# Kernel tuning notes

Measured on AMD Instinct MI355X. Metric: run time of the kernel, lower is better.

The kernel has to match this reference:

```python
import jax, jax.numpy as jnp
import numpy as np

EPS = 1e-5  # BatchNorm eps
K = 10      # knn neighbors

def mish(x):
    return x * jnp.tanh(jax.nn.softplus(x))

def block(h, w, g, b, m, v):
    # 1x1 conv (no bias) + BN (inference stats) + Mish; h: [..., Cin], w: [Cout, Cin]
    y = jnp.einsum('...c,oc->...o', h, w)
    y = (y - m) * (g * jax.lax.rsqrt(v + EPS)) + b
    return mish(y)

def graph_feature(xt, k):
    # xt: [B, N, C] -> edge features [B, N, k, 2C] = cat(neighbor - center, center)
    xx = jnp.sum(xt * xt, axis=-1)                       # [B,N]
    inner = jnp.einsum('bnc,bmc->bnm', xt, xt)           # [B,N,N]
    neg_dist = 2.0 * inner - xx[:, :, None] - xx[:, None, :]
    idx = jax.lax.top_k(neg_dist, k)[1]                  # [B,N,k] nearest (incl. self)
    feat = jax.vmap(lambda a, i: a[i])(xt, idx)          # [B,N,k,C]
    center = jnp.broadcast_to(xt[:, :, None, :], feat.shape)
    return jnp.concatenate([feat - center, center], axis=-1)

def _bn_params(key, c):
    k1, k2, k3, k4 = jax.random.split(key, 4)
    g = 1.0 + 0.1 * jax.random.normal(k1, (c,), jnp.float32)
    b = 0.1 * jax.random.normal(k2, (c,), jnp.float32)
    m = 0.1 * jax.random.normal(k3, (c,), jnp.float32)
    v = 0.5 + jax.random.uniform(k4, (c,), jnp.float32)
    return g, b, m, v

def setup_inputs() -> dict:
    key = jax.random.key(0)
    B, C, N = 4, 3, 4096
    emb = 1024
    ks = jax.random.split(key, 20)
    d = {'x': jax.random.normal(ks[0], (B, C, N), jnp.float32)}
    dims = {'1': (64, 2 * C), '2': (64, 64), '3': (64, 128), '4': (64, 64),
            '6': (emb, 128), '7': (512, emb + 128), '8': (256, 512)}
    i = 1
    for name, (co, ci) in dims.items():
        d['w' + name] = jax.random.normal(ks[i], (co, ci), jnp.float32) * (1.0 / np.sqrt(ci))
        g, b, m, v = _bn_params(ks[i + 1], co)
        d['g' + name], d['b' + name], d['m' + name], d['v' + name] = g, b, m, v
        i += 2
    d['w9'] = jax.random.normal(ks[i], (2, 256), jnp.float32) * (1.0 / np.sqrt(256))
    return d

def reference(x, w1, g1, b1, m1, v1, w2, g2, b2, m2, v2, w3, g3, b3, m3, v3,
              w4, g4, b4, m4, v4, w6, g6, b6, m6, v6, w7, g7, b7, m7, v7,
              w8, g8, b8, m8, v8, w9):
    B, C, N = x.shape
    xt = jnp.transpose(x, (0, 2, 1))                    # [B,N,3]
    ef = graph_feature(xt, K)                           # [B,N,k,6]
    h = block(block(ef, w1, g1, b1, m1, v1), w2, g2, b2, m2, v2)
    x1 = jnp.max(h, axis=2)                             # [B,N,64]
    ef = graph_feature(x1, K)                           # [B,N,k,128]
    h = block(block(ef, w3, g3, b3, m3, v3), w4, g4, b4, m4, v4)
    x2 = jnp.max(h, axis=2)                             # [B,N,64]
    cat = jnp.concatenate([x1, x2], axis=-1)            # [B,N,128]
    h6 = block(cat, w6, g6, b6, m6, v6)                 # [B,N,1024]
    gmax = jnp.max(h6, axis=1, keepdims=True)           # [B,1,1024]
    gb = jnp.broadcast_to(gmax, (B, N, gmax.shape[-1]))
    cat2 = jnp.concatenate([gb, x1, x2], axis=-1)       # [B,N,1152]
    h = block(block(cat2, w7, g7, b7, m7, v7), w8, g8, b8, m8, v8)
    out = jnp.einsum('bnc,oc->bon', h, w9)              # [B,2,N]
    return out
```

## Files before the change

kernel.cpp:

```cpp
#include <hip/hip_runtime.h>
#include <cfloat>


#define BN_EPS 1e-5f

__device__ __forceinline__ float mish_f(float x) {
  float e = __expf(x);
  float num = e * (e + 2.0f);
  float r = x * (num / (num + 2.0f));
  return (x > 44.0f) ? x : r;
}

__device__ __forceinline__ float rl_f(float v, int l) {
  return __uint_as_float((unsigned)__builtin_amdgcn_readlane((int)__float_as_uint(v), l));
}

__device__ __forceinline__ unsigned enc_f(float f) {
  unsigned b = __float_as_uint(f);
  return (b & 0x80000000u) ? ~b : (b | 0x80000000u);
}
__device__ __forceinline__ float dec_f(unsigned u) {
  unsigned b = (u & 0x80000000u) ? (u ^ 0x80000000u) : ~u;
  return __uint_as_float(b);
}

__device__ __forceinline__ void topk_insert(float (&v)[10], int (&id)[10], float nd, int m) {
  if (nd > v[9]) {
    v[9] = nd; id[9] = m;
#pragma unroll
    for (int j = 9; j > 0; --j) {
      if (v[j] > v[j - 1]) {
        float tv = v[j]; v[j] = v[j - 1]; v[j - 1] = tv;
        int ti = id[j]; id[j] = id[j - 1]; id[j - 1] = ti;
      }
    }
  }
}

__global__ __launch_bounds__(256) void knn1_k(const float* __restrict__ x, int* __restrict__ idx1) {
  __shared__ float pls[3][4100];
  const int tid = threadIdx.x;
  const int rowBase = blockIdx.x * 64;
  const int b = rowBase >> 12;
  const float* xb = x + (size_t)b * 3 * 4096;
#pragma unroll
  for (int c = 0; c < 3; ++c) {
#pragma unroll
    for (int s = 0; s < 16; ++s) {
      int li = tid + 256 * s;
      pls[c][(li >> 10) * 1025 + (li & 1023)] = xb[c * 4096 + li];
    }
  }
  __syncthreads();
  const int sub = tid & 3;
  const int nloc = (rowBase & 4095) + (tid >> 2);
  float pnx = xb[nloc], pny = xb[4096 + nloc], pnz = xb[8192 + nloc];
  float xxn = pnx * pnx; xxn = fmaf(pny, pny, xxn); xxn = fmaf(pnz, pnz, xxn);
  float v[10]; int id[10];
#pragma unroll
  for (int j = 0; j < 10; ++j) { v[j] = -FLT_MAX; id[j] = -1; }
  const int base = sub * 1025;
  for (int i = 0; i < 1024; ++i) {
    float mx = pls[0][base + i], my = pls[1][base + i], mz = pls[2][base + i];
    float in = mx * pnx; in = fmaf(my, pny, in); in = fmaf(mz, pnz, in);
    float xm = mx * mx;  xm = fmaf(my, my, xm);  xm = fmaf(mz, mz, xm);
    float nd = 2.0f * in - xxn - xm;
    topk_insert(v, id, nd, sub * 1024 + i);
  }
  int k0 = -1, k1 = -1, k2 = -1;
#pragma unroll
  for (int r = 0; r < 10; ++r) {
    float mv = v[0]; int mi = id[0];
    { float ov = __shfl_xor(mv, 1); int oi = __shfl_xor(mi, 1);
      if (ov > mv || (ov == mv && oi < mi)) { mv = ov; mi = oi; } }
    { float ov = __shfl_xor(mv, 2); int oi = __shfl_xor(mi, 2);
      if (ov > mv || (ov == mv && oi < mi)) { mv = ov; mi = oi; } }
    if (id[0] == mi) {
#pragma unroll
      for (int j = 0; j < 9; ++j) { v[j] = v[j + 1]; id[j] = id[j + 1]; }
      v[9] = -FLT_MAX; id[9] = -1;
    }
    if ((r & 3) == sub) { if (r < 4) k0 = mi; else if (r < 8) k1 = mi; else k2 = mi; }
  }
  const int obase = (rowBase + (tid >> 2)) * 10;
  if (sub == 0)      { idx1[obase + 0] = k0; idx1[obase + 4] = k1; idx1[obase + 8] = k2; }
  else if (sub == 1) { idx1[obase + 1] = k0; idx1[obase + 5] = k1; idx1[obase + 9] = k2; }
  else if (sub == 2) { idx1[obase + 2] = k0; idx1[obase + 6] = k1; }
  else               { idx1[obase + 3] = k0; idx1[obase + 7] = k1; }
}

__global__ __launch_bounds__(256) void pre1_k(const float* __restrict__ x, const float* __restrict__ w1,
                                              float* __restrict__ e1m, float* __restrict__ e1n) {
  int gt = blockIdx.x * 256 + threadIdx.x;
  int pt = gt >> 6, c = gt & 63;
  int b = pt >> 12, n = pt & 4095;
  const float* xb = x + (size_t)b * 3 * 4096;
  float px = xb[n], py = xb[4096 + n], pz = xb[8192 + n];
  const float* wr = w1 + c * 6;
  float a0 = wr[0], a1 = wr[1], a2 = wr[2], b0 = wr[3], b1 = wr[4], b2 = wr[5];
  float vm = a0 * px; vm = fmaf(a1, py, vm); vm = fmaf(a2, pz, vm);
  float un = (b0 - a0) * px; un = fmaf(b1 - a1, py, un); un = fmaf(b2 - a2, pz, un);
  e1m[(size_t)pt * 64 + c] = vm;
  e1n[(size_t)pt * 64 + c] = un;
}

template <bool WRITE_XX>
__global__ __launch_bounds__(256) void edge_k(
    const int* __restrict__ idx,
    const float* __restrict__ vm, const float* __restrict__ un, int stride,
    const float* __restrict__ w,
    const float* __restrict__ ga, const float* __restrict__ ba, const float* __restrict__ ma, const float* __restrict__ va,
    const float* __restrict__ gb, const float* __restrict__ bb, const float* __restrict__ mb, const float* __restrict__ vb,
    float* __restrict__ outCat, int outOff, float* __restrict__ xxOut) {
  const int tid = threadIdx.x;
  const int wid = tid >> 6, lane = tid & 63;
  const int r = blockIdx.x * 4 + wid;
  const int mbase = (r >> 12) << 12;
  float4 wv[16];
  const float4* wp = (const float4*)(w + lane * 64);
#pragma unroll
  for (int i = 0; i < 16; ++i) wv[i] = wp[i];
  float s1 = ga[lane] * rsqrtf(va[lane] + BN_EPS); float t1 = ba[lane] - ma[lane] * s1;
  float s2 = gb[lane] * rsqrtf(vb[lane] + BN_EPS); float t2 = bb[lane] - mb[lane] * s2;
  float uc = un[(size_t)r * stride + lane];
  float best = -FLT_MAX;
#pragma unroll
  for (int kk = 0; kk < 10; ++kk) {
    int m = idx[r * 10 + kk];
    float pre = vm[(size_t)(mbase + m) * stride + lane] + uc;
    float h1 = mish_f(fmaf(pre, s1, t1));
    float acc = 0.f;
#pragma unroll
    for (int j4 = 0; j4 < 16; ++j4) {
      float4 wq = wv[j4];
      acc = fmaf(wq.x, rl_f(h1, 4 * j4 + 0), acc);
      acc = fmaf(wq.y, rl_f(h1, 4 * j4 + 1), acc);
      acc = fmaf(wq.z, rl_f(h1, 4 * j4 + 2), acc);
      acc = fmaf(wq.w, rl_f(h1, 4 * j4 + 3), acc);
    }
    float h2 = mish_f(fmaf(acc, s2, t2));
    best = fmaxf(best, h2);
  }
  outCat[(size_t)r * 128 + outOff + lane] = best;
  if (WRITE_XX) {
    float q = best * best;
#pragma unroll
    for (int o = 1; o < 64; o <<= 1) q += __shfl_xor(q, o);
    if (lane == 0) xxOut[r] = q;
  }
}

#define KNN2_CHUNKS 16
__global__ __launch_bounds__(256, 4) void knn2_k(const float* __restrict__ cat,
                                                 const float* __restrict__ xx2,
                                                 float* __restrict__ pv, int* __restrict__ pi) {
  __shared__ float tile[128 * 68];
  __shared__ float xxm[128];
  const int tid = threadIdx.x;
  const int r = blockIdx.x * 256 + tid;
  const int nbase = (r >> 12) << 12;
  const int cb = blockIdx.y * 256;
  float4 q[16];
  const float4* qp = (const float4*)(cat + (size_t)r * 128);
#pragma unroll
  for (int s = 0; s < 16; ++s) q[s] = qp[s];
  const float xxA = xx2[r];
  float v[10]; int id[10];
#pragma unroll
  for (int j = 0; j < 10; ++j) { v[j] = -FLT_MAX; id[j] = -1; }
  for (int t = 0; t < 2; ++t) {
    __syncthreads();
    {
      const int m = tid >> 1, h = tid & 1;
      const float4* src = (const float4*)(cat + (size_t)(nbase + cb + t * 128 + m) * 128) + h * 8;
      float4* dst = (float4*)(tile + m * 68) + h * 8;
#pragma unroll
      for (int s = 0; s < 8; ++s) dst[s] = src[s];
      if (tid < 128) xxm[tid] = xx2[nbase + cb + t * 128 + tid];
    }
    __syncthreads();
    for (int m = 0; m < 128; ++m) {
      const float4* crow = (const float4*)(tile + m * 68);
      float a0 = 0.f, a1 = 0.f, a2 = 0.f, a3 = 0.f;
#pragma unroll
      for (int c4 = 0; c4 < 16; c4 += 4) {
        float4 t0 = crow[c4 + 0], t1 = crow[c4 + 1], t2 = crow[c4 + 2], t3 = crow[c4 + 3];
        a0 = fmaf(t0.x, q[c4 + 0].x, a0); a0 = fmaf(t0.y, q[c4 + 0].y, a0);
        a0 = fmaf(t0.z, q[c4 + 0].z, a0); a0 = fmaf(t0.w, q[c4 + 0].w, a0);
        a1 = fmaf(t1.x, q[c4 + 1].x, a1); a1 = fmaf(t1.y, q[c4 + 1].y, a1);
        a1 = fmaf(t1.z, q[c4 + 1].z, a1); a1 = fmaf(t1.w, q[c4 + 1].w, a1);
        a2 = fmaf(t2.x, q[c4 + 2].x, a2); a2 = fmaf(t2.y, q[c4 + 2].y, a2);
        a2 = fmaf(t2.z, q[c4 + 2].z, a2); a2 = fmaf(t2.w, q[c4 + 2].w, a2);
        a3 = fmaf(t3.x, q[c4 + 3].x, a3); a3 = fmaf(t3.y, q[c4 + 3].y, a3);
        a3 = fmaf(t3.z, q[c4 + 3].z, a3); a3 = fmaf(t3.w, q[c4 + 3].w, a3);
      }
      float nd = 2.0f * ((a0 + a1) + (a2 + a3)) - xxA - xxm[m];
      topk_insert(v, id, nd, cb + t * 128 + m);
    }
  }
  const size_t ob = ((size_t)blockIdx.y * 16384 + r) * 10;
#pragma unroll
  for (int j = 0; j < 10; ++j) { pv[ob + j] = v[j]; pi[ob + j] = id[j]; }
}

__global__ __launch_bounds__(256) void knn2m_k(const float* __restrict__ pv,
                                               const int* __restrict__ pi,
                                               int* __restrict__ idx2) {
  const int r = blockIdx.x * 256 + threadIdx.x;
  float v[10]; int id[10];
#pragma unroll
  for (int j = 0; j < 10; ++j) { v[j] = -FLT_MAX; id[j] = -1; }
  for (int c = 0; c < KNN2_CHUNKS; ++c) {
    const size_t base = ((size_t)c * 16384 + r) * 10;
    if (pv[base] > v[9]) {
#pragma unroll
      for (int j = 0; j < 10; ++j) topk_insert(v, id, pv[base + j], pi[base + j]);
    }
  }
#pragma unroll
  for (int j = 0; j < 10; ++j) idx2[r * 10 + j] = id[j];
}

__global__ void w3s_k(const float* __restrict__ w3, float* __restrict__ w3s) {
  int t = blockIdx.x * 256 + threadIdx.x;
  int c = t >> 6, k = t & 63;
  float v;
  if (c < 64) v = w3[c * 128 + k];
  else { int cc = c - 64; v = w3[cc * 128 + 64 + k] - w3[cc * 128 + k]; }
  w3s[t] = v;
}

template <int QM, int QN, int EPI>
__global__ __launch_bounds__(256) void gemm_k(
    const float* __restrict__ A, int lda,
    const float* __restrict__ W, int ldw,
    float* __restrict__ C, int ldc, int K, int Ntot,
    const float* __restrict__ eg, const float* __restrict__ eb,
    const float* __restrict__ em, const float* __restrict__ ev,
    const float* __restrict__ pbBias, unsigned int* __restrict__ gmaxOut) {
  constexpr int BM = 64 * QM, BN = 64 * QN;
  __shared__ float aL[16][BM];
  __shared__ float bL[16][BN];
  __shared__ unsigned int cm[BN];
  const int tid = threadIdx.x;
  const int tm = tid >> 4, tn = tid & 15;
  const int rowBase = blockIdx.x * BM;
  const int colBase = blockIdx.y * BN;
  float acc[QM][QN][4][4] = {};
  if (EPI == 2 && tid < BN) cm[tid] = 0u;
  const int nkt = K >> 4;
  for (int kt = 0; kt < nkt; ++kt) {
#pragma unroll
    for (int s = 0; s < QM; ++s) {
      int fi = tid + 256 * s;
      int m = fi >> 2, k4 = fi & 3;
      float4 t4 = *(const float4*)(A + (size_t)(rowBase + m) * lda + (kt << 4) + k4 * 4);
      aL[k4 * 4 + 0][m] = t4.x; aL[k4 * 4 + 1][m] = t4.y;
      aL[k4 * 4 + 2][m] = t4.z; aL[k4 * 4 + 3][m] = t4.w;
    }
#pragma unroll
    for (int s = 0; s < QN; ++s) {
      int fi = tid + 256 * s;
      int n = fi >> 2, k4 = fi & 3;
      float4 t4 = *(const float4*)(W + (size_t)(colBase + n) * ldw + (kt << 4) + k4 * 4);
      bL[k4 * 4 + 0][n] = t4.x; bL[k4 * 4 + 1][n] = t4.y;
      bL[k4 * 4 + 2][n] = t4.z; bL[k4 * 4 + 3][n] = t4.w;
    }
    __syncthreads();
#pragma unroll
    for (int k = 0; k < 16; ++k) {
      float ar[QM][4], br[QN][4];
#pragma unroll
      for (int q = 0; q < QM; ++q) {
        float4 t4 = *(const float4*)&aL[k][q * 64 + tm * 4];
        ar[q][0] = t4.x; ar[q][1] = t4.y; ar[q][2] = t4.z; ar[q][3] = t4.w;
      }
#pragma unroll
      for (int q = 0; q < QN; ++q) {
        float4 t4 = *(const float4*)&bL[k][q * 64 + tn * 4];
        br[q][0] = t4.x; br[q][1] = t4.y; br[q][2] = t4.z; br[q][3] = t4.w;
      }
#pragma unroll
      for (int qm = 0; qm < QM; ++qm)
#pragma unroll
        for (int qn = 0; qn < QN; ++qn)
#pragma unroll
          for (int i = 0; i < 4; ++i)
#pragma unroll
            for (int j = 0; j < 4; ++j)
              acc[qm][qn][i][j] = fmaf(ar[qm][i], br[qn][j], acc[qm][qn][i][j]);
    }
    __syncthreads();
  }
  if (EPI == 0) {
#pragma unroll
    for (int qm = 0; qm < QM; ++qm)
#pragma unroll
      for (int i = 0; i < 4; ++i) {
        int row = rowBase + qm * 64 + tm * 4 + i;
#pragma unroll
        for (int qn = 0; qn < QN; ++qn) {
          float4 o;
          o.x = acc[qm][qn][i][0]; o.y = acc[qm][qn][i][1];
          o.z = acc[qm][qn][i][2]; o.w = acc[qm][qn][i][3];
          *(float4*)(C + (size_t)row * ldc + colBase + qn * 64 + tn * 4) = o;
        }
      }
  } else {
    const int bidx = rowBase >> 12;
    float sc[QN][4], sh[QN][4];
#pragma unroll
    for (int qn = 0; qn < QN; ++qn)
#pragma unroll
      for (int j = 0; j < 4; ++j) {
        int cg = colBase + qn * 64 + tn * 4 + j;
        float s = eg[cg] * rsqrtf(ev[cg] + BN_EPS);
        sc[qn][j] = s;
        sh[qn][j] = (EPI == 3) ? pbBias[bidx * Ntot + cg] : (eb[cg] - em[cg] * s);
      }
    if (EPI == 2) {
      float cmax[QN][4];
#pragma unroll
      for (int qn = 0; qn < QN; ++qn)
#pragma unroll
        for (int j = 0; j < 4; ++j) cmax[qn][j] = -FLT_MAX;
#pragma unroll
      for (int qm = 0; qm < QM; ++qm)
#pragma unroll
        for (int qn = 0; qn < QN; ++qn)
#pragma unroll
          for (int i = 0; i < 4; ++i)
#pragma unroll
            for (int j = 0; j < 4; ++j) {
              float vv = mish_f(fmaf(acc[qm][qn][i][j], sc[qn][j], sh[qn][j]));
              cmax[qn][j] = fmaxf(cmax[qn][j], vv);
            }
#pragma unroll
      for (int qn = 0; qn < QN; ++qn)
#pragma unroll
        for (int j = 0; j < 4; ++j)
          atomicMax(&cm[qn * 64 + tn * 4 + j], enc_f(cmax[qn][j]));
      __syncthreads();
      if (tid < BN) atomicMax(&gmaxOut[bidx * Ntot + colBase + tid], cm[tid]);
    } else {
#pragma unroll
      for (int qm = 0; qm < QM; ++qm)
#pragma unroll
        for (int i = 0; i < 4; ++i) {
          int row = rowBase + qm * 64 + tm * 4 + i;
#pragma unroll
          for (int qn = 0; qn < QN; ++qn) {
            float4 o;
            o.x = mish_f(fmaf(acc[qm][qn][i][0], sc[qn][0], sh[qn][0]));
            o.y = mish_f(fmaf(acc[qm][qn][i][1], sc[qn][1], sh[qn][1]));
            o.z = mish_f(fmaf(acc[qm][qn][i][2], sc[qn][2], sh[qn][2]));
            o.w = mish_f(fmaf(acc[qm][qn][i][3], sc[qn][3], sh[qn][3]));
            *(float4*)(C + (size_t)row * ldc + colBase + qn * 64 + tn * 4) = o;
          }
        }
    }
  }
}

__global__ __launch_bounds__(256) void bias7_k(const unsigned int* __restrict__ gmaxU,
                                               const float* __restrict__ w7,
                                               const float* __restrict__ g7, const float* __restrict__ b7,
                                               const float* __restrict__ m7, const float* __restrict__ v7,
                                               float* __restrict__ bias7) {
  __shared__ float gl[1024];
  const int tid = threadIdx.x;
  const int batch = blockIdx.x >> 1, half = blockIdx.x & 1;
#pragma unroll
  for (int s = 0; s < 4; ++s) gl[tid + 256 * s] = dec_f(gmaxU[batch * 1024 + tid + 256 * s]);
  __syncthreads();
  const int ch = half * 256 + tid;
  const float4* wr = (const float4*)(w7 + (size_t)ch * 1152);
  float acc = 0.f;
  for (int j4 = 0; j4 < 256; ++j4) {
    float4 w = wr[j4];
    float4 g = *(const float4*)&gl[j4 * 4];
    acc = fmaf(w.x, g.x, acc); acc = fmaf(w.y, g.y, acc);
    acc = fmaf(w.z, g.z, acc); acc = fmaf(w.w, g.w, acc);
  }
  float s7 = g7[ch] * rsqrtf(v7[ch] + BN_EPS);
  bias7[batch * 512 + ch] = acc * s7 + (b7[ch] - m7[ch] * s7);
}

__global__ __launch_bounds__(256) void out_k(const float* __restrict__ h8,
                                             const float* __restrict__ w9, float* __restrict__ out) {
  __shared__ float w9l[512];
  const int tid = threadIdx.x;
  w9l[tid] = w9[tid];
  w9l[256 + tid] = w9[256 + tid];
  __syncthreads();
  const int t = blockIdx.x * 256 + tid;
  const int b = t >> 12, n = t & 4095;
  const float4* hr = (const float4*)(h8 + (size_t)t * 256);
  float a0 = 0.f, a1 = 0.f;
#pragma unroll
  for (int j4 = 0; j4 < 64; ++j4) {
    float4 h = hr[j4];
    float4 wa = *(const float4*)&w9l[j4 * 4];
    float4 wb = *(const float4*)&w9l[256 + j4 * 4];
    a0 = fmaf(h.x, wa.x, a0); a0 = fmaf(h.y, wa.y, a0);
    a0 = fmaf(h.z, wa.z, a0); a0 = fmaf(h.w, wa.w, a0);
    a1 = fmaf(h.x, wb.x, a1); a1 = fmaf(h.y, wb.y, a1);
    a1 = fmaf(h.z, wb.z, a1); a1 = fmaf(h.w, wb.w, a1);
  }
  out[(size_t)b * 8192 + n] = a0;
  out[(size_t)b * 8192 + 4096 + n] = a1;
}

extern "C" void kernel_launch(void* const* d_in, const int* in_sizes, int n_in,
                              void* d_out, int out_size, void* d_ws, size_t ws_size,
                              hipStream_t stream) {
  const float* x  = (const float*)d_in[0];
  const float* w1 = (const float*)d_in[1];
  const float* g1 = (const float*)d_in[2];
  const float* b1 = (const float*)d_in[3];
  const float* m1 = (const float*)d_in[4];
  const float* v1 = (const float*)d_in[5];
  const float* w2 = (const float*)d_in[6];
  const float* g2 = (const float*)d_in[7];
  const float* b2 = (const float*)d_in[8];
  const float* m2 = (const float*)d_in[9];
  const float* v2 = (const float*)d_in[10];
  const float* w3 = (const float*)d_in[11];
  const float* g3 = (const float*)d_in[12];
  const float* b3 = (const float*)d_in[13];
  const float* m3 = (const float*)d_in[14];
  const float* v3 = (const float*)d_in[15];
  const float* w4 = (const float*)d_in[16];
  const float* g4 = (const float*)d_in[17];
  const float* b4 = (const float*)d_in[18];
  const float* m4 = (const float*)d_in[19];
  const float* v4 = (const float*)d_in[20];
  const float* w6 = (const float*)d_in[21];
  const float* g6 = (const float*)d_in[22];
  const float* b6 = (const float*)d_in[23];
  const float* m6 = (const float*)d_in[24];
  const float* v6 = (const float*)d_in[25];
  const float* w7 = (const float*)d_in[26];
  const float* g7 = (const float*)d_in[27];
  const float* b7 = (const float*)d_in[28];
  const float* m7 = (const float*)d_in[29];
  const float* v7 = (const float*)d_in[30];
  const float* w8 = (const float*)d_in[31];
  const float* g8 = (const float*)d_in[32];
  const float* b8 = (const float*)d_in[33];
  const float* m8 = (const float*)d_in[34];
  const float* v8 = (const float*)d_in[35];
  const float* w9 = (const float*)d_in[36];

  float* ws = (float*)d_ws;
  int* idx1       = (int*)(ws + 0);
  int* idx2       = (int*)(ws + 163840);
  float* xx2      = ws + 327680;
  unsigned* gmax  = (unsigned*)(ws + 344064);
  float* bias7    = ws + 348160;
  float* w3s      = ws + 350208;
  float* e1n      = ws + 358400;
  float* e1m      = ws + 1406976;
  float* pre3     = ws + 358400;
  float* cat      = ws + 2455552;
  float* h7       = ws + 4552704;
  float* h8       = ws + 12941312;
  float* knn2pv   = h7;
  int*   knn2pi   = (int*)(h7 + 2621440);

  hipMemsetAsync(gmax, 0, 4096 * sizeof(unsigned), stream);

  knn1_k<<<256, 256, 0, stream>>>(x, idx1);
  pre1_k<<<4096, 256, 0, stream>>>(x, w1, e1m, e1n);
  edge_k<true><<<4096, 256, 0, stream>>>(idx1, e1m, e1n, 64, w2,
                                         g1, b1, m1, v1, g2, b2, m2, v2,
                                         cat, 0, xx2);
  w3s_k<<<32, 256, 0, stream>>>(w3, w3s);
  gemm_k<1, 2, 0><<<dim3(256, 1), 256, 0, stream>>>(cat, 128, w3s, 64, pre3, 128, 64, 0,
                                                    nullptr, nullptr, nullptr, nullptr, nullptr, nullptr);
  knn2_k<<<dim3(64, KNN2_CHUNKS), 256, 0, stream>>>(cat, xx2, knn2pv, knn2pi);
  knn2m_k<<<64, 256, 0, stream>>>(knn2pv, knn2pi, idx2);
  edge_k<false><<<4096, 256, 0, stream>>>(idx2, pre3, pre3 + 64, 128, w4,
                                          g3, b3, m3, v3, g4, b4, m4, v4,
                                          cat, 64, nullptr);
  gemm_k<2, 2, 2><<<dim3(128, 8), 256, 0, stream>>>(cat, 128, w6, 128, nullptr, 0, 128, 1024,
                                                    g6, b6, m6, v6, nullptr, gmax);
  bias7_k<<<8, 256, 0, stream>>>(gmax, w7, g7, b7, m7, v7, bias7);
  gemm_k<2, 2, 3><<<dim3(128, 4), 256, 0, stream>>>(cat, 128, w7 + 1024, 1152, h7, 512, 128, 512,
                                                    g7, nullptr, nullptr, v7, bias7, nullptr);
  gemm_k<1, 2, 1><<<dim3(256, 2), 256, 0, stream>>>(h7, 512, w8, 512, h8, 256, 512, 256,
                                                    g8, b8, m8, v8, nullptr, nullptr);
  out_k<<<64, 256, 0, stream>>>(h8, w9, (float*)d_out);
}
```

Before: 1.046 ms.

## Drop LDS tiling in knn2, read candidates directly, use branchless top-k

The knn2 kernel no longer stages candidate rows and their squared norms into shared memory with barriers. Each thread now reads the candidate rows straight from global memory; the reads are wavefront-uniform, so they can be served as broadcast/scalar loads. The top-k insertion becomes a branchless select network, and the launch-bound occupancy hint drops from 4 to 2 to give more registers. The aim is to remove LDS traffic, syncs and divergent insertion branches, at the cost of relying on cache and fewer resident waves.

```diff
diff --git a/kernel.cpp b/kernel.cpp
--- a/kernel.cpp
+++ b/kernel.cpp
@@ -35,6 +35,19 @@
       }
     }
   }
+}
+
+__device__ __forceinline__ void topk_bl(float (&v)[10], int (&id)[10], float nd, int m) {
+  bool c[10];
+#pragma unroll
+  for (int j = 0; j < 10; ++j) c[j] = nd > v[j];
+#pragma unroll
+  for (int j = 9; j >= 1; --j) {
+    v[j]  = c[j - 1] ? v[j - 1]  : (c[j] ? nd : v[j]);
+    id[j] = c[j - 1] ? id[j - 1] : (c[j] ? m  : id[j]);
+  }
+  v[0]  = c[0] ? nd : v[0];
+  id[0] = c[0] ? m  : id[0];
 }
 
 __global__ __launch_bounds__(256) void knn1_k(const float* __restrict__ x, int* __restrict__ idx1) {
@@ -151,11 +164,9 @@
 }
 
 #define KNN2_CHUNKS 16
-__global__ __launch_bounds__(256, 4) void knn2_k(const float* __restrict__ cat,
+__global__ __launch_bounds__(256, 2) void knn2_k(const float* __restrict__ cat,
                                                  const float* __restrict__ xx2,
                                                  float* __restrict__ pv, int* __restrict__ pi) {
-  __shared__ float tile[128 * 68];
-  __shared__ float xxm[128];
   const int tid = threadIdx.x;
   const int r = blockIdx.x * 256 + tid;
   const int nbase = (r >> 12) << 12;
@@ -168,35 +179,27 @@
   float v[10]; int id[10];
 #pragma unroll
   for (int j = 0; j < 10; ++j) { v[j] = -FLT_MAX; id[j] = -1; }
-  for (int t = 0; t < 2; ++t) {
-    __syncthreads();
-    {
-      const int m = tid >> 1, h = tid & 1;
-      const float4* src = (const float4*)(cat + (size_t)(nbase + cb + t * 128 + m) * 128) + h * 8;
-      float4* dst = (float4*)(tile + m * 68) + h * 8;
-#pragma unroll
-      for (int s = 0; s < 8; ++s) dst[s] = src[s];
-      if (tid < 128) xxm[tid] = xx2[nbase + cb + t * 128 + tid];
-    }
-    __syncthreads();
-    for (int m = 0; m < 128; ++m) {
-      const float4* crow = (const float4*)(tile + m * 68);
-      float a0 = 0.f, a1 = 0.f, a2 = 0.f, a3 = 0.f;
-#pragma unroll
-      for (int c4 = 0; c4 < 16; c4 += 4) {
-        float4 t0 = crow[c4 + 0], t1 = crow[c4 + 1], t2 = crow[c4 + 2], t3 = crow[c4 + 3];
-        a0 = fmaf(t0.x, q[c4 + 0].x, a0); a0 = fmaf(t0.y, q[c4 + 0].y, a0);
-        a0 = fmaf(t0.z, q[c4 + 0].z, a0); a0 = fmaf(t0.w, q[c4 + 0].w, a0);
-        a1 = fmaf(t1.x, q[c4 + 1].x, a1); a1 = fmaf(t1.y, q[c4 + 1].y, a1);
-        a1 = fmaf(t1.z, q[c4 + 1].z, a1); a1 = fmaf(t1.w, q[c4 + 1].w, a1);
-        a2 = fmaf(t2.x, q[c4 + 2].x, a2); a2 = fmaf(t2.y, q[c4 + 2].y, a2);
-        a2 = fmaf(t2.z, q[c4 + 2].z, a2); a2 = fmaf(t2.w, q[c4 + 2].w, a2);
-        a3 = fmaf(t3.x, q[c4 + 3].x, a3); a3 = fmaf(t3.y, q[c4 + 3].y, a3);
-        a3 = fmaf(t3.z, q[c4 + 3].z, a3); a3 = fmaf(t3.w, q[c4 + 3].w, a3);
-      }
-      float nd = 2.0f * ((a0 + a1) + (a2 + a3)) - xxA - xxm[m];
-      topk_insert(v, id, nd, cb + t * 128 + m);
-    }
+
+  const float* __restrict__ crow = cat + (size_t)(nbase + cb) * 128;
+  const float* __restrict__ xxp = xx2 + nbase + cb;
+#pragma unroll 2
+  for (int m = 0; m < 256; ++m) {
+    const float4* cr4 = (const float4*)(crow + (size_t)m * 128);
+    float a0 = 0.f, a1 = 0.f, a2 = 0.f, a3 = 0.f;
+#pragma unroll
+    for (int c4 = 0; c4 < 16; c4 += 4) {
+      float4 t0 = cr4[c4 + 0], t1 = cr4[c4 + 1], t2 = cr4[c4 + 2], t3 = cr4[c4 + 3];
+      a0 = fmaf(t0.x, q[c4 + 0].x, a0); a0 = fmaf(t0.y, q[c4 + 0].y, a0);
+      a0 = fmaf(t0.z, q[c4 + 0].z, a0); a0 = fmaf(t0.w, q[c4 + 0].w, a0);
+      a1 = fmaf(t1.x, q[c4 + 1].x, a1); a1 = fmaf(t1.y, q[c4 + 1].y, a1);
+      a1 = fmaf(t1.z, q[c4 + 1].z, a1); a1 = fmaf(t1.w, q[c4 + 1].w, a1);
+      a2 = fmaf(t2.x, q[c4 + 2].x, a2); a2 = fmaf(t2.y, q[c4 + 2].y, a2);
+      a2 = fmaf(t2.z, q[c4 + 2].z, a2); a2 = fmaf(t2.w, q[c4 + 2].w, a2);
+      a3 = fmaf(t3.x, q[c4 + 3].x, a3); a3 = fmaf(t3.y, q[c4 + 3].y, a3);
+      a3 = fmaf(t3.z, q[c4 + 3].z, a3); a3 = fmaf(t3.w, q[c4 + 3].w, a3);
+    }
+    float nd = 2.0f * ((a0 + a1) + (a2 + a3)) - xxA - xxp[m];
+    topk_bl(v, id, nd, cb + m);
   }
   const size_t ob = ((size_t)blockIdx.y * 16384 + r) * 10;
 #pragma unroll
```

New measurement: 1.622 ms. 1.55x slower.
